# Kernel optimization log

Hardware: AMD Instinct MI355X
Metric: run time of the kernel (lower is better)

Reference implementation:

```python
import jax, jax.numpy as jnp
import numpy as np

N = 50000   # nodes
R = 3       # relations
E = 300000  # edges per relation
H, D = 4, 32  # heads, per-head dim (hidden_feat=128)
IN, HID, OUT = 128, 128, 64
SLOPE = 0.2  # DGL GATConv leaky_relu negative slope


def setup_inputs() -> dict:
    key = jax.random.key(0)
    ks = jax.random.split(key, 12)
    s = 0.05
    return {
        "x": jax.random.normal(ks[0], (N, IN), jnp.float32),
        "edges": jax.random.randint(ks[1], (R, 2, E), 0, N, jnp.int64),
        "W1": jax.random.normal(ks[2], (R, IN, H * D), jnp.float32) * s,
        "al1": jax.random.normal(ks[3], (R, H, D), jnp.float32) * s,
        "ar1": jax.random.normal(ks[4], (R, H, D), jnp.float32) * s,
        "b1": jnp.zeros((R, H, D), jnp.float32),
        "W2": jax.random.normal(ks[5], (R, HID, H * D), jnp.float32) * s,
        "al2": jax.random.normal(ks[6], (R, H, D), jnp.float32) * s,
        "ar2": jax.random.normal(ks[7], (R, H, D), jnp.float32) * s,
        "b2": jnp.zeros((R, H, D), jnp.float32),
        "Wl": jax.random.normal(ks[8], (HID, OUT), jnp.float32) * s,
        "bl": jnp.zeros((OUT,), jnp.float32),
    }


def rgat_layer(h, edges, W, al, ar, b):
    """HeteroGraphConv(sum) of per-relation GATConv. h: [N,F]. Returns [N,H,D]."""
    out = jnp.zeros((N, H, D), h.dtype)
    for r in range(R):  # small fixed relation count
        src, dst = edges[r, 0], edges[r, 1]
        feat = (h @ W[r]).reshape(N, H, D)                  # per-relation projection
        el = jnp.einsum("nhd,hd->nh", feat, al[r])          # [N,H]
        er = jnp.einsum("nhd,hd->nh", feat, ar[r])          # [N,H]
        e = jax.nn.leaky_relu(el[src] + er[dst], SLOPE)      # [E,H]
        # edge softmax over incoming edges per destination node
        emax = jax.ops.segment_max(e, dst, num_segments=N)   # [N,H]
        ex = jnp.exp(e - emax[dst])
        denom = jax.ops.segment_sum(ex, dst, num_segments=N) # [N,H]
        alpha = ex / denom[dst]                               # [E,H]
        msg = feat[src] * alpha[:, :, None]                   # [E,H,D]
        out = out + jax.ops.segment_sum(msg, dst, num_segments=N) + b[r]
    return out


def reference(x, edges, W1, al1, ar1, b1, W2, al2, ar2, b2, Wl, bl):
    h = rgat_layer(x, edges, W1, al1, ar1, b1).reshape(N, H * D)
    h = jax.nn.relu(h)  # dropout is identity in eval mode
    h = rgat_layer(h, edges, W2, al2, ar2, b2).reshape(N, H * D)
    return h @ Wl + bl  # [N, OUT]
```

## Files before the change

kernel.cpp:

```cpp
#include <hip/hip_runtime.h>
#include <hip/hip_bf16.h>
#include <hip/hip_fp16.h>

#define Nn 50000
#define RR 3
#define EE 300000

typedef __attribute__((ext_vector_type(8))) short short8;
typedef __attribute__((ext_vector_type(4))) short short4v;
typedef __attribute__((ext_vector_type(4))) float floatx4;

__device__ __forceinline__ short f2bf(float f) {
    __hip_bfloat16 h = __float2bfloat16(f);
    return *reinterpret_cast<short*>(&h);
}


__global__ void init_kernel(const float* __restrict__ W1, const float* __restrict__ W2,
                            short* __restrict__ Z, int* __restrict__ counts,
                            int* __restrict__ totals) {
    int bx = blockIdx.x;
    if (bx < 586) {
        int i = bx * 256 + threadIdx.x;
        if (i < RR * Nn) counts[i] = 0;
        if (i < 4) totals[i] = 0;
    } else {
        int idx = (bx - 586) * 256 + threadIdx.x;
        if (idx >= 12288) return;
        int lane = idx & 63;
        int nt = (idx >> 6) & 7;
        int kt = (idx >> 9) & 3;
        int rl = idx >> 11;
        int layer = rl / 3, r = rl % 3;
        const float* W = (layer ? W2 : W1) + (size_t)r * 16384;
        int n = nt * 16 + (lane & 15);
        int k0 = kt * 32 + (lane >> 4) * 8;
        short8 v;
        #pragma unroll
        for (int j = 0; j < 8; ++j) v[j] = f2bf(W[(size_t)(k0 + j) * 128 + n]);
        *(short8*)&Z[(size_t)idx * 8] = v;
    }
}


__global__ void count_kernel(const int* __restrict__ edges, int* __restrict__ counts,
                             int* __restrict__ ord) {
    int i = blockIdx.x * blockDim.x + threadIdx.x;
    if (i >= RR * EE / 8) return;
    int g = i * 8;
    int r = g / EE, e0 = g - r * EE;
    const int* db = &edges[(size_t)r * 2 * EE + EE + e0];
    int4 d0 = *(const int4*)db;
    int4 d1 = *(const int4*)(db + 4);
    int* cb = counts + r * Nn;
    int4 o0, o1;
    o0.x = atomicAdd(&cb[d0.x], 1);
    o0.y = atomicAdd(&cb[d0.y], 1);
    o0.z = atomicAdd(&cb[d0.z], 1);
    o0.w = atomicAdd(&cb[d0.w], 1);
    o1.x = atomicAdd(&cb[d1.x], 1);
    o1.y = atomicAdd(&cb[d1.y], 1);
    o1.z = atomicAdd(&cb[d1.z], 1);
    o1.w = atomicAdd(&cb[d1.w], 1);
    *(int4*)&ord[g] = o0;
    *(int4*)&ord[g + 4] = o1;
}

__global__ __launch_bounds__(256) void alloc_kernel(const int* __restrict__ counts,
                                                    int* __restrict__ row_start,
                                                    int* __restrict__ totals) {
    __shared__ int s[256];
    __shared__ int base_s;
    int r = blockIdx.y;
    int tid = threadIdx.x;
    int n = blockIdx.x * 256 + tid;
    int idx = r * Nn + n;
    int c = (n < Nn) ? counts[idx] : 0;
    s[tid] = c;
    __syncthreads();
    #pragma unroll
    for (int off = 1; off < 256; off <<= 1) {
        int v = 0;
        if (tid >= off) v = s[tid - off];
        __syncthreads();
        if (tid >= off) s[tid] += v;
        __syncthreads();
    }
    if (tid == 255) base_s = atomicAdd(&totals[r], s[255]);
    __syncthreads();
    if (n < Nn) row_start[idx] = base_s + s[tid] - c;
}

__global__ void scatter_kernel(const int* __restrict__ edges, const int* __restrict__ ord,
                               const int* __restrict__ row_start,
                               int* __restrict__ csr_s, int* __restrict__ csr_d) {
    int i = blockIdx.x * blockDim.x + threadIdx.x;
    if (i >= RR * EE / 8) return;
    int g = i * 8;
    int r = g / EE, e0 = g - r * EE;
    const int* sb = &edges[(size_t)r * 2 * EE + e0];
    const int* db = sb + EE;
    int4 s0 = *(const int4*)sb, s1 = *(const int4*)(sb + 4);
    int4 d0 = *(const int4*)db, d1 = *(const int4*)(db + 4);
    int4 o0 = *(const int4*)&ord[g], o1 = *(const int4*)&ord[g + 4];
    const int* rs = row_start + r * Nn;
    int* cs = csr_s + (size_t)r * EE;
    int* cd = csr_d + (size_t)r * EE;
    int p0 = rs[d0.x] + o0.x, p1 = rs[d0.y] + o0.y;
    int p2 = rs[d0.z] + o0.z, p3 = rs[d0.w] + o0.w;
    int p4 = rs[d1.x] + o1.x, p5 = rs[d1.y] + o1.y;
    int p6 = rs[d1.z] + o1.z, p7 = rs[d1.w] + o1.w;
    cs[p0] = s0.x; cs[p1] = s0.y; cs[p2] = s0.z; cs[p3] = s0.w;
    cs[p4] = s1.x; cs[p5] = s1.y; cs[p6] = s1.z; cs[p7] = s1.w;
    cd[p0] = d0.x; cd[p1] = d0.y; cd[p2] = d0.z; cd[p3] = d0.w;
    cd[p4] = d1.x; cd[p5] = d1.y; cd[p6] = d1.z; cd[p7] = d1.w;
}


template<bool RELU_A>
__global__ __launch_bounds__(256) void gemm_proj_mfma(const float* __restrict__ A,
                                                      const short* __restrict__ Z,
                                                      const float* __restrict__ al,
                                                      const float* __restrict__ ar,
                                                      __half* __restrict__ C,
                                                      float* __restrict__ el,
                                                      float* __restrict__ er) {
    __shared__ short A_lds[64 * 136];
    __shared__ float al_lds[384], ar_lds[384];
    int tid = threadIdx.x;
    int row0 = blockIdx.x * 64;
    if (tid < 128) { al_lds[256 + tid] = al[256 + tid]; ar_lds[256 + tid] = ar[256 + tid]; }
    al_lds[tid] = al[tid]; ar_lds[tid] = ar[tid];
    #pragma unroll
    for (int p = 0; p < 8; ++p) {
        int f = p * 256 + tid;
        int row = f >> 5;
        int c4 = (f & 31) * 4;
        float4 v = make_float4(0.f, 0.f, 0.f, 0.f);
        if (row0 + row < Nn) v = *(const float4*)&A[(size_t)(row0 + row) * 128 + c4];
        if (RELU_A) {
            v.x = fmaxf(v.x, 0.f); v.y = fmaxf(v.y, 0.f);
            v.z = fmaxf(v.z, 0.f); v.w = fmaxf(v.w, 0.f);
        }
        short4v sv;
        sv[0] = f2bf(v.x); sv[1] = f2bf(v.y); sv[2] = f2bf(v.z); sv[3] = f2bf(v.w);
        *(short4v*)&A_lds[row * 136 + c4] = sv;
    }
    __syncthreads();
    int wave = tid >> 6, lane = tid & 63;
    int m = lane & 15, q = lane >> 4;
    short8 af[4];
    #pragma unroll
    for (int kt = 0; kt < 4; ++kt)
        af[kt] = *(short8*)&A_lds[(wave * 16 + m) * 136 + kt * 32 + q * 8];
    __syncthreads();
    __half* lds_h = (__half*)A_lds;
    int row8 = tid >> 2;
    int hh = tid & 3;
    for (int r = 0; r < RR; ++r) {
        floatx4 acc[8];
        #pragma unroll
        for (int nt = 0; nt < 8; ++nt) acc[nt] = (floatx4)(0.f);
        const short* Zr = Z + (size_t)r * 16384;
        #pragma unroll
        for (int kt = 0; kt < 4; ++kt) {
            #pragma unroll
            for (int nt = 0; nt < 8; ++nt) {
                short8 bf = *(const short8*)&Zr[(size_t)(kt * 8 + nt) * 512 + lane * 8];
                acc[nt] = __builtin_amdgcn_mfma_f32_16x16x32_bf16(af[kt], bf, acc[nt], 0, 0, 0);
            }
        }
        #pragma unroll
        for (int nt = 0; nt < 8; ++nt) {
            int col = nt * 16 + m;
            #pragma unroll
            for (int reg = 0; reg < 4; ++reg)
                lds_h[(wave * 16 + q * 4 + reg) * 136 + col] = __float2half(acc[nt][reg]);
        }
        __syncthreads();
        __half* Cr = C + (size_t)r * Nn * 128;
        #pragma unroll
        for (int p = 0; p < 4; ++p) {
            int lin = p * 256 + tid;
            int row = lin >> 4, c8 = (lin & 15) * 8;
            if (row0 + row < Nn)
                *(short8*)&Cr[(size_t)(row0 + row) * 128 + c8] = *(short8*)&lds_h[row * 136 + c8];
        }
        {
            const __half2* fp = (const __half2*)&lds_h[row8 * 136 + hh * 32];
            const float* alp = &al_lds[r * 128 + hh * 32];
            const float* arp = &ar_lds[r * 128 + hh * 32];
            float sl = 0.f, sr = 0.f;
            #pragma unroll
            for (int d = 0; d < 16; ++d) {
                float2 v = __half22float2(fp[d]);
                sl += v.x * alp[2 * d] + v.y * alp[2 * d + 1];
                sr += v.x * arp[2 * d] + v.y * arp[2 * d + 1];
            }
            if (row0 + row8 < Nn) {
                size_t ei = (size_t)(r * Nn + row0 + row8) * 4 + hh;
                el[ei] = sl;
                er[ei] = sr;
            }
        }
        __syncthreads();
    }
}


__global__ __launch_bounds__(256) void gemm_final_kernel(const float* __restrict__ A,
                                                         const float* __restrict__ Wl,
                                                         const float* __restrict__ bl,
                                                         float* __restrict__ out) {
    __shared__ float As[16][65];
    __shared__ float Bs[16][65];
    int tid = threadIdx.x;
    int row0 = blockIdx.x * 64;
    float acc[4][4] = {};
    int tx = tid & 15, ty = tid >> 4;
    for (int k0 = 0; k0 < 128; k0 += 16) {
        {
            int mm = tid >> 2, c = (tid & 3) * 4;
            int row = row0 + mm;
            float4 v = make_float4(0.f, 0.f, 0.f, 0.f);
            if (row < Nn) v = *(const float4*)&A[(size_t)row * 128 + k0 + c];
            As[c + 0][mm] = v.x; As[c + 1][mm] = v.y; As[c + 2][mm] = v.z; As[c + 3][mm] = v.w;
        }
        {
            int kk = tid >> 4, j = (tid & 15) * 4;
            float4 v = *(const float4*)&Wl[(size_t)(k0 + kk) * 64 + j];
            *(float4*)&Bs[kk][j] = v;
        }
        __syncthreads();
        #pragma unroll
        for (int kk = 0; kk < 16; ++kk) {
            float4 a = *(const float4*)&As[kk][ty * 4];
            float4 b = *(const float4*)&Bs[kk][tx * 4];
            float av[4] = {a.x, a.y, a.z, a.w};
            float bv[4] = {b.x, b.y, b.z, b.w};
            #pragma unroll
            for (int i = 0; i < 4; ++i)
                #pragma unroll
                for (int j = 0; j < 4; ++j) acc[i][j] += av[i] * bv[j];
        }
        __syncthreads();
    }
    float4 bias = *(const float4*)&bl[tx * 4];
    #pragma unroll
    for (int i = 0; i < 4; ++i) {
        int row = row0 + ty * 4 + i;
        if (row >= Nn) continue;
        float4 v = make_float4(acc[i][0] + bias.x, acc[i][1] + bias.y,
                               acc[i][2] + bias.z, acc[i][3] + bias.w);
        *(float4*)&out[(size_t)row * 64 + tx * 4] = v;
    }
}


__global__ __launch_bounds__(256) void wexp_kernel(const int* __restrict__ csr_s,
                                                   const int* __restrict__ csr_d,
                                                   const float* __restrict__ el,
                                                   const float* __restrict__ er,
                                                   float* __restrict__ wq) {
    int r = blockIdx.y;
    int k = blockIdx.x * 256 + threadIdx.x;
    if (k >= EE) return;
    size_t gk = (size_t)r * EE + k;
    int es = csr_s[gk], ed = csr_d[gk];
    float4 l4 = *(const float4*)&el[(size_t)(r * Nn + es) * 4];
    float4 r4 = *(const float4*)&er[(size_t)(r * Nn + ed) * 4];
    float lv[4] = {l4.x, l4.y, l4.z, l4.w};
    float rv[4] = {r4.x, r4.y, r4.z, r4.w};
    #pragma unroll
    for (int h = 0; h < 4; ++h) {
        float x = lv[h] + rv[h];
        x = (x > 0.f) ? x : 0.2f * x;
        wq[(size_t)h * (RR * EE) + gk] = __expf(x);
    }
}


__global__ __launch_bounds__(256) void agg_kernel(const __half2* __restrict__ feat2,
                                                  const float* __restrict__ wq,
                                                  const int* __restrict__ csr_s,
                                                  const int* __restrict__ row_start,
                                                  const int* __restrict__ counts,
                                                  const float* __restrict__ b,
                                                  float* __restrict__ out) {
    int wave = threadIdx.x >> 6;
    int lane = threadIdx.x & 63;
    int n = blockIdx.x * 4 + wave;
    if (n >= Nn) return;
    int h = lane >> 4;
    int hl = lane & 15;
    int grp = lane & 48;
    int t2 = lane * 2;
    int cntA[RR], stA[RR], sC[RR];
    float wC[RR];
    #pragma unroll
    for (int r = 0; r < RR; ++r) {
        cntA[r] = counts[r * Nn + n];
        stA[r] = row_start[r * Nn + n];
    }
    #pragma unroll
    for (int r = 0; r < RR; ++r) {
        sC[r] = 0; wC[r] = 0.f;
        if (hl < cntA[r]) {
            int idx = stA[r] + hl;
            sC[r] = csr_s[(size_t)r * EE + idx];
            wC[r] = wq[(size_t)h * (RR * EE) + (size_t)r * EE + idx];
        }
    }
    float accx = b[t2] + b[128 + t2] + b[256 + t2];
    float accy = b[t2 + 1] + b[128 + t2 + 1] + b[256 + t2 + 1];
    #pragma unroll
    for (int r = 0; r < RR; ++r) {
        int cnt = cntA[r];
        if (cnt == 0) continue;
        const __half2* fr = feat2 + (size_t)r * Nn * 64;
        float den = 0.f, numx = 0.f, numy = 0.f;
        int s_l = sC[r];
        float w_l = wC[r];
        int i0 = 0;
        while (true) {
            int mm = cnt - i0; if (mm > 16) mm = 16;
            int mm4 = (mm + 3) & ~3;
            for (int j = 0; j < mm4; j += 4) {
                int s0 = __shfl(s_l, j);
                int s1 = __shfl(s_l, j + 1);
                int s2 = __shfl(s_l, j + 2);
                int s3 = __shfl(s_l, j + 3);
                float w0 = __shfl(w_l, grp | j);
                float w1 = __shfl(w_l, grp | (j + 1));
                float w2 = __shfl(w_l, grp | (j + 2));
                float w3 = __shfl(w_l, grp | (j + 3));
                __half2 f0 = fr[(size_t)s0 * 64 + lane];
                __half2 f1 = fr[(size_t)s1 * 64 + lane];
                __half2 f2 = fr[(size_t)s2 * 64 + lane];
                __half2 f3 = fr[(size_t)s3 * 64 + lane];
                float2 g0 = __half22float2(f0), g1 = __half22float2(f1);
                float2 g2 = __half22float2(f2), g3 = __half22float2(f3);
                den += (w0 + w1) + (w2 + w3);
                numx += w0 * g0.x + w1 * g1.x + w2 * g2.x + w3 * g3.x;
                numy += w0 * g0.y + w1 * g1.y + w2 * g2.y + w3 * g3.y;
            }
            i0 += 16;
            if (i0 >= cnt) break;
            s_l = 0; w_l = 0.f;
            if (i0 + hl < cnt) {
                int idx = stA[r] + i0 + hl;
                s_l = csr_s[(size_t)r * EE + idx];
                w_l = wq[(size_t)h * (RR * EE) + (size_t)r * EE + idx];
            }
        }
        float inv = 1.f / den;
        accx += numx * inv;
        accy += numy * inv;
    }
    *(float2*)&out[(size_t)n * 128 + t2] = make_float2(accx, accy);
}


extern "C" void kernel_launch(void* const* d_in, const int* in_sizes, int n_in,
                              void* d_out, int out_size, void* d_ws, size_t ws_size,
                              hipStream_t stream) {
    const float* x   = (const float*)d_in[0];
    const int*  edges = (const int*)d_in[1];
    const float* W1  = (const float*)d_in[2];
    const float* al1 = (const float*)d_in[3];
    const float* ar1 = (const float*)d_in[4];
    const float* b1  = (const float*)d_in[5];
    const float* W2  = (const float*)d_in[6];
    const float* al2 = (const float*)d_in[7];
    const float* ar2 = (const float*)d_in[8];
    const float* b2  = (const float*)d_in[9];
    const float* Wl  = (const float*)d_in[10];
    const float* bl  = (const float*)d_in[11];
    float* out = (float*)d_out;

    __half* feat  = (__half*)d_ws;
    short* Z      = (short*)(feat + (size_t)RR * Nn * 128);
    float* el     = (float*)(Z + 98304);
    float* er     = el + (size_t)RR * Nn * 4;
    float* outbuf = er + (size_t)RR * Nn * 4;
    float* wq     = outbuf + (size_t)Nn * 128;
    int* counts    = (int*)(wq + (size_t)4 * RR * EE);
    int* row_start = counts + RR * Nn;
    int* totals    = row_start + RR * Nn;
    int* ord       = totals + 4;
    int* csr_s     = ord + RR * EE;
    int* csr_d     = csr_s + RR * EE;

    const int rowBlocks  = (Nn + 63) / 64;
    const int nodeBlocks = (Nn + 255) / 256;
    const int aggBlocks  = (Nn + 3) / 4;
    const int edgeBlocks = (EE + 255) / 256;
    const int edge8Blocks = (RR * EE / 8 + 255) / 256;

    init_kernel<<<634, 256, 0, stream>>>(W1, W2, Z, counts, totals);
    count_kernel<<<edge8Blocks, 256, 0, stream>>>(edges, counts, ord);
    alloc_kernel<<<dim3(nodeBlocks, RR), 256, 0, stream>>>(counts, row_start, totals);
    scatter_kernel<<<edge8Blocks, 256, 0, stream>>>(edges, ord, row_start, csr_s, csr_d);

    gemm_proj_mfma<false><<<rowBlocks, 256, 0, stream>>>(x, Z, al1, ar1, feat, el, er);
    wexp_kernel<<<dim3(edgeBlocks, RR), 256, 0, stream>>>(csr_s, csr_d, el, er, wq);
    agg_kernel<<<aggBlocks, 256, 0, stream>>>((const __half2*)feat, wq, csr_s, row_start, counts, b1, outbuf);

    gemm_proj_mfma<true><<<rowBlocks, 256, 0, stream>>>(outbuf, Z + 49152, al2, ar2, feat, el, er);
    wexp_kernel<<<dim3(edgeBlocks, RR), 256, 0, stream>>>(csr_s, csr_d, el, er, wq);
    agg_kernel<<<aggBlocks, 256, 0, stream>>>((const __half2*)feat, wq, csr_s, row_start, counts, b2, outbuf);

    gemm_final_kernel<<<rowBlocks, 256, 0, stream>>>(outbuf, Wl, bl, out);
}
```

Baseline: 343.9 us.

## Store edge weights in fp16, emit layer-1 output as bf16, unroll aggregation by 8

Edge attention weights are now stored as fp16 instead of fp32, which halves that buffer's write and read traffic. The first aggregation applies ReLU and writes bf16 directly, so the second projection GEMM loads bf16 rows without converting them. The aggregation inner loop is unrolled from 4 to 8 gathers to allow more loads in flight. The cost is lower precision in the softmax weights and the intermediate hidden state, plus more wasted padded iterations for nodes with low degree.

Measured after the change: 337.7 us. About the same (-1.8%).

```diff
diff --git a/kernel.cpp b/kernel.cpp
--- a/kernel.cpp
+++ b/kernel.cpp
@@ -1,6 +1,7 @@
 #include <hip/hip_runtime.h>
 #include <hip/hip_bf16.h>
 #include <hip/hip_fp16.h>
+#include <type_traits>
 
 #define Nn 50000
 #define RR 3
@@ -13,6 +14,10 @@
 __device__ __forceinline__ short f2bf(float f) {
     __hip_bfloat16 h = __float2bfloat16(f);
     return *reinterpret_cast<short*>(&h);
+}
+__device__ __forceinline__ float bf2f(short s) {
+    __hip_bfloat16 h = *reinterpret_cast<__hip_bfloat16*>(&s);
+    return __bfloat162float(h);
 }
 
 
@@ -117,8 +122,8 @@
 }
 
 
-template<bool RELU_A>
-__global__ __launch_bounds__(256) void gemm_proj_mfma(const float* __restrict__ A,
+template<typename TA>
+__global__ __launch_bounds__(256) void gemm_proj_mfma(const TA* __restrict__ A,
                                                       const short* __restrict__ Z,
                                                       const float* __restrict__ al,
                                                       const float* __restrict__ ar,
@@ -131,20 +136,27 @@
     int row0 = blockIdx.x * 64;
     if (tid < 128) { al_lds[256 + tid] = al[256 + tid]; ar_lds[256 + tid] = ar[256 + tid]; }
     al_lds[tid] = al[tid]; ar_lds[tid] = ar[tid];
-    #pragma unroll
-    for (int p = 0; p < 8; ++p) {
-        int f = p * 256 + tid;
-        int row = f >> 5;
-        int c4 = (f & 31) * 4;
-        float4 v = make_float4(0.f, 0.f, 0.f, 0.f);
-        if (row0 + row < Nn) v = *(const float4*)&A[(size_t)(row0 + row) * 128 + c4];
-        if (RELU_A) {
-            v.x = fmaxf(v.x, 0.f); v.y = fmaxf(v.y, 0.f);
-            v.z = fmaxf(v.z, 0.f); v.w = fmaxf(v.w, 0.f);
-        }
-        short4v sv;
-        sv[0] = f2bf(v.x); sv[1] = f2bf(v.y); sv[2] = f2bf(v.z); sv[3] = f2bf(v.w);
-        *(short4v*)&A_lds[row * 136 + c4] = sv;
+    if constexpr (std::is_same<TA, float>::value) {
+        #pragma unroll
+        for (int p = 0; p < 8; ++p) {
+            int f = p * 256 + tid;
+            int row = f >> 5;
+            int c4 = (f & 31) * 4;
+            float4 v = make_float4(0.f, 0.f, 0.f, 0.f);
+            if (row0 + row < Nn) v = *(const float4*)&A[(size_t)(row0 + row) * 128 + c4];
+            short4v sv;
+            sv[0] = f2bf(v.x); sv[1] = f2bf(v.y); sv[2] = f2bf(v.z); sv[3] = f2bf(v.w);
+            *(short4v*)&A_lds[row * 136 + c4] = sv;
+        }
+    } else {
+        #pragma unroll
+        for (int p = 0; p < 4; ++p) {
+            int c = p * 256 + tid;
+            int row = c >> 4, c8 = (c & 15) * 8;
+            short8 v = (short8)(0);
+            if (row0 + row < Nn) v = *(const short8*)&A[(size_t)(row0 + row) * 128 + c8];
+            *(short8*)&A_lds[row * 136 + c8] = v;
+        }
     }
     __syncthreads();
     int wave = tid >> 6, lane = tid & 63;
@@ -261,7 +273,7 @@
                                                    const int* __restrict__ csr_d,
                                                    const float* __restrict__ el,
                                                    const float* __restrict__ er,
-                                                   float* __restrict__ wq) {
+                                                   __half* __restrict__ wq) {
     int r = blockIdx.y;
     int k = blockIdx.x * 256 + threadIdx.x;
     if (k >= EE) return;
@@ -275,18 +287,19 @@
     for (int h = 0; h < 4; ++h) {
         float x = lv[h] + rv[h];
         x = (x > 0.f) ? x : 0.2f * x;
-        wq[(size_t)h * (RR * EE) + gk] = __expf(x);
-    }
-}
-
-
+        wq[(size_t)h * (RR * EE) + gk] = __float2half(__expf(x));
+    }
+}
+
+
+template<bool OUT_BF16_RELU>
 __global__ __launch_bounds__(256) void agg_kernel(const __half2* __restrict__ feat2,
-                                                  const float* __restrict__ wq,
+                                                  const __half* __restrict__ wq,
                                                   const int* __restrict__ csr_s,
                                                   const int* __restrict__ row_start,
                                                   const int* __restrict__ counts,
                                                   const float* __restrict__ b,
-                                                  float* __restrict__ out) {
+                                                  void* __restrict__ out) {
     int wave = threadIdx.x >> 6;
     int lane = threadIdx.x & 63;
     int n = blockIdx.x * 4 + wave;
@@ -308,7 +321,7 @@
         if (hl < cntA[r]) {
             int idx = stA[r] + hl;
             sC[r] = csr_s[(size_t)r * EE + idx];
-            wC[r] = wq[(size_t)h * (RR * EE) + (size_t)r * EE + idx];
+            wC[r] = __half2float(wq[(size_t)h * (RR * EE) + (size_t)r * EE + idx]);
         }
     }
     float accx = b[t2] + b[128 + t2] + b[256 + t2];
@@ -324,25 +337,41 @@
         int i0 = 0;
         while (true) {
             int mm = cnt - i0; if (mm > 16) mm = 16;
-            int mm4 = (mm + 3) & ~3;
-            for (int j = 0; j < mm4; j += 4) {
+            int mm8 = (mm + 7) & ~7;
+            for (int j = 0; j < mm8; j += 8) {
                 int s0 = __shfl(s_l, j);
                 int s1 = __shfl(s_l, j + 1);
                 int s2 = __shfl(s_l, j + 2);
                 int s3 = __shfl(s_l, j + 3);
+                int s4 = __shfl(s_l, j + 4);
+                int s5 = __shfl(s_l, j + 5);
+                int s6 = __shfl(s_l, j + 6);
+                int s7 = __shfl(s_l, j + 7);
                 float w0 = __shfl(w_l, grp | j);
                 float w1 = __shfl(w_l, grp | (j + 1));
                 float w2 = __shfl(w_l, grp | (j + 2));
                 float w3 = __shfl(w_l, grp | (j + 3));
+                float w4 = __shfl(w_l, grp | (j + 4));
+                float w5 = __shfl(w_l, grp | (j + 5));
+                float w6 = __shfl(w_l, grp | (j + 6));
+                float w7 = __shfl(w_l, grp | (j + 7));
                 __half2 f0 = fr[(size_t)s0 * 64 + lane];
                 __half2 f1 = fr[(size_t)s1 * 64 + lane];
                 __half2 f2 = fr[(size_t)s2 * 64 + lane];
                 __half2 f3 = fr[(size_t)s3 * 64 + lane];
+                __half2 f4 = fr[(size_t)s4 * 64 + lane];
+                __half2 f5 = fr[(size_t)s5 * 64 + lane];
+                __half2 f6 = fr[(size_t)s6 * 64 + lane];
+                __half2 f7 = fr[(size_t)s7 * 64 + lane];
                 float2 g0 = __half22float2(f0), g1 = __half22float2(f1);
                 float2 g2 = __half22float2(f2), g3 = __half22float2(f3);
-                den += (w0 + w1) + (w2 + w3);
-                numx += w0 * g0.x + w1 * g1.x + w2 * g2.x + w3 * g3.x;
-                numy += w0 * g0.y + w1 * g1.y + w2 * g2.y + w3 * g3.y;
+                float2 g4 = __half22float2(f4), g5 = __half22float2(f5);
+                float2 g6 = __half22float2(f6), g7 = __half22float2(f7);
+                den += ((w0 + w1) + (w2 + w3)) + ((w4 + w5) + (w6 + w7));
+                numx += (w0 * g0.x + w1 * g1.x + w2 * g2.x + w3 * g3.x)
+                      + (w4 * g4.x + w5 * g5.x + w6 * g6.x + w7 * g7.x);
+                numy += (w0 * g0.y + w1 * g1.y + w2 * g2.y + w3 * g3.y)
+                      + (w4 * g4.y + w5 * g5.y + w6 * g6.y + w7 * g7.y);
             }
             i0 += 16;
             if (i0 >= cnt) break;
@@ -350,14 +379,23 @@
             if (i0 + hl < cnt) {
                 int idx = stA[r] + i0 + hl;
                 s_l = csr_s[(size_t)r * EE + idx];
-                w_l = wq[(size_t)h * (RR * EE) + (size_t)r * EE + idx];
+                w_l = __half2float(wq[(size_t)h * (RR * EE) + (size_t)r * EE + idx]);
             }
         }
         float inv = 1.f / den;
         accx += numx * inv;
         accy += numy * inv;
     }
-    *(float2*)&out[(size_t)n * 128 + t2] = make_float2(accx, accy);
+    if constexpr (OUT_BF16_RELU) {
+        short* o = (short*)out;
+        short2 pk;
+        pk.x = f2bf(fmaxf(accx, 0.f));
+        pk.y = f2bf(fmaxf(accy, 0.f));
+        *(short2*)&o[(size_t)n * 128 + t2] = pk;
+    } else {
+        float* o = (float*)out;
+        *(float2*)&o[(size_t)n * 128 + t2] = make_float2(accx, accy);
+    }
 }
 
 
@@ -383,13 +421,14 @@
     float* el     = (float*)(Z + 98304);
     float* er     = el + (size_t)RR * Nn * 4;
     float* outbuf = er + (size_t)RR * Nn * 4;
-    float* wq     = outbuf + (size_t)Nn * 128;
+    __half* wq    = (__half*)(outbuf + (size_t)Nn * 128);
     int* counts    = (int*)(wq + (size_t)4 * RR * EE);
     int* row_start = counts + RR * Nn;
     int* totals    = row_start + RR * Nn;
     int* ord       = totals + 4;
     int* csr_s     = ord + RR * EE;
     int* csr_d     = csr_s + RR * EE;
+    short* outb16  = (short*)outbuf;
 
     const int rowBlocks  = (Nn + 63) / 64;
     const int nodeBlocks = (Nn + 255) / 256;
@@ -402,13 +441,13 @@
     alloc_kernel<<<dim3(nodeBlocks, RR), 256, 0, stream>>>(counts, row_start, totals);
     scatter_kernel<<<edge8Blocks, 256, 0, stream>>>(edges, ord, row_start, csr_s, csr_d);
 
-    gemm_proj_mfma<false><<<rowBlocks, 256, 0, stream>>>(x, Z, al1, ar1, feat, el, er);
+    gemm_proj_mfma<float><<<rowBlocks, 256, 0, stream>>>(x, Z, al1, ar1, feat, el, er);
     wexp_kernel<<<dim3(edgeBlocks, RR), 256, 0, stream>>>(csr_s, csr_d, el, er, wq);
-    agg_kernel<<<aggBlocks, 256, 0, stream>>>((const __half2*)feat, wq, csr_s, row_start, counts, b1, outbuf);
-
-    gemm_proj_mfma<true><<<rowBlocks, 256, 0, stream>>>(outbuf, Z + 49152, al2, ar2, feat, el, er);
+    agg_kernel<true><<<aggBlocks, 256, 0, stream>>>((const __half2*)feat, wq, csr_s, row_start, counts, b1, outb16);
+
+    gemm_proj_mfma<short><<<rowBlocks, 256, 0, stream>>>(outb16, Z + 49152, al2, ar2, feat, el, er);
     wexp_kernel<<<dim3(edgeBlocks, RR), 256, 0, stream>>>(csr_s, csr_d, el, er, wq);
-    agg_kernel<<<aggBlocks, 256, 0, stream>>>((const __half2*)feat, wq, csr_s, row_start, counts, b2, outbuf);
+    agg_kernel<false><<<aggBlocks, 256, 0, stream>>>((const __half2*)feat, wq, csr_s, row_start, counts, b2, outbuf);
 
     gemm_final_kernel<<<rowBlocks, 256, 0, stream>>>(outbuf, Wl, bl, out);
 }
```
